# Kernel tuning notes

Measured on AMD Instinct MI355X. Metric: run time of the kernel, lower is better.

Reference implementation:

```python
import jax, jax.numpy as jnp
import numpy as np
from jax import lax


def _gelu(x):
    return jax.nn.gelu(x, approximate=False)  # torch nn.GELU default = exact erf


def _ln_cf(x, g, b, eps=1e-6):
    # channels_first LayerNorm over dim 1 (biased variance, as in the source)
    m = x.mean(1, keepdims=True)
    v = ((x - m) ** 2).mean(1, keepdims=True)
    return g[None, :, None, None] * ((x - m) / jnp.sqrt(v + eps)) + b[None, :, None, None]


def _conv1x1(x, w):
    return jnp.einsum('bihw,oi->bohw', x, w[:, :, 0, 0])


def _conv3x3(x, w, d):
    # 3x3 conv, padding=dilation=d, no bias
    return lax.conv_general_dilated(x, w, (1, 1), [(d, d), (d, d)], rhs_dilation=(d, d),
                                    dimension_numbers=('NCHW', 'OIHW', 'NCHW'))


def _forward(x, conv1_w, conv1_b, conv2_w, conv2_b,
             cw_w1, cw_b1, cw_ln_g, cw_ln_b, cw_w2, cw_b2,
             aspp0_w, aspp0_g, aspp0_b, aspp1_w, aspp1_g, aspp1_b,
             aspp2_w, aspp2_g, aspp2_b, aspp3_w, aspp3_g, aspp3_b,
             asppp_w, asppp_g, asppp_b, proj_w, proj_g, proj_b):
    B, C, H, W = x.shape
    # x1 = conv1(x)
    x1 = _conv1x1(x, conv1_w) + conv1_b[None, :, None, None]
    # ChannelWeighting
    avg = x.mean((2, 3))                                    # [B,C]
    mx = x.max((2, 3))
    o = jnp.abs(avg - mx) * avg
    h = o @ cw_w1.T + cw_b1                                 # [B,Cout]
    mu = h.mean(-1, keepdims=True)
    vv = ((h - mu) ** 2).mean(-1, keepdims=True)
    h = cw_ln_g * ((h - mu) / jnp.sqrt(vv + 1e-5)) + cw_ln_b  # nn.LayerNorm eps=1e-5
    s = jax.nn.sigmoid(h @ cw_w2.T + cw_b2)                 # [B,C]
    xc = x * s[:, :, None, None] + x
    # ASPP (dropout in project is identity at eval)
    b0 = _gelu(_ln_cf(_conv1x1(xc, aspp0_w), aspp0_g, aspp0_b))
    b1 = _gelu(_ln_cf(_conv3x3(xc, aspp1_w, 3), aspp1_g, aspp1_b))
    b2 = _gelu(_ln_cf(_conv3x3(xc, aspp2_w, 6), aspp2_g, aspp2_b))
    b3 = _gelu(_ln_cf(_conv3x3(xc, aspp3_w, 9), aspp3_g, aspp3_b))
    gp = xc.mean((2, 3), keepdims=True)                     # AdaptiveAvgPool2d(1)
    bp = _gelu(_ln_cf(_conv1x1(gp, asppp_w), asppp_g, asppp_b))
    bp = jnp.broadcast_to(bp, (B, C, H, W))                 # bilinear 1x1->HxW == broadcast
    cat = jnp.concatenate([b0, b1, b2, b3, bp], axis=1)     # [B,5C,H,W]
    proj = _gelu(_ln_cf(_conv1x1(cat, proj_w), proj_g, proj_b))
    xa = _conv1x1(proj, conv1_w) + conv1_b[None, :, None, None]
    # AttentionModule, batched (redundant discarded Q@attn from source omitted)
    Co = xa.shape[1]
    HW = H * W
    P = x1.reshape(B, Co, HW)
    Q = xa.reshape(B, Co, HW)
    S = jnp.einsum('bcq,bcp->bqp', Q, P) / jnp.sqrt(jnp.asarray(HW, jnp.float32))
    A = jax.nn.softmax(S, axis=-1)                          # softmax over dim=1 of S[q,p] -> p
    L = jnp.einsum('bck,bkj->bcj', P, A).reshape(B, Co, H, W)
    O = L + xa
    return _conv1x1(O, conv2_w) + conv2_b[None, :, None, None]


def setup_inputs() -> dict:
    key = jax.random.key(0)
    ks = jax.random.split(key, 16)
    Cin, Cout, B, H, W = 256, 128, 4, 64, 64

    def nrm(k, shape, fan):
        return jax.random.normal(k, shape, jnp.float32) / np.float32(np.sqrt(fan))

    return {
        'x': jax.random.normal(ks[0], (B, Cin, H, W), jnp.float32),
        'conv1_w': nrm(ks[1], (Cout, Cin, 1, 1), Cin),
        'conv1_b': jnp.zeros((Cout,), jnp.float32),
        'conv2_w': nrm(ks[2], (Cin, Cout, 1, 1), Cout),
        'conv2_b': jnp.zeros((Cin,), jnp.float32),
        'cw_w1': nrm(ks[3], (Cout, Cin), Cin),
        'cw_b1': jnp.zeros((Cout,), jnp.float32),
        'cw_ln_g': jnp.ones((Cout,), jnp.float32),
        'cw_ln_b': jnp.zeros((Cout,), jnp.float32),
        'cw_w2': nrm(ks[4], (Cin, Cout), Cout),
        'cw_b2': jnp.zeros((Cin,), jnp.float32),
        'aspp0_w': nrm(ks[5], (Cin, Cin, 1, 1), Cin),
        'aspp0_g': jnp.ones((Cin,), jnp.float32),
        'aspp0_b': jnp.zeros((Cin,), jnp.float32),
        'aspp1_w': nrm(ks[6], (Cin, Cin, 3, 3), Cin * 9),
        'aspp1_g': jnp.ones((Cin,), jnp.float32),
        'aspp1_b': jnp.zeros((Cin,), jnp.float32),
        'aspp2_w': nrm(ks[7], (Cin, Cin, 3, 3), Cin * 9),
        'aspp2_g': jnp.ones((Cin,), jnp.float32),
        'aspp2_b': jnp.zeros((Cin,), jnp.float32),
        'aspp3_w': nrm(ks[8], (Cin, Cin, 3, 3), Cin * 9),
        'aspp3_g': jnp.ones((Cin,), jnp.float32),
        'aspp3_b': jnp.zeros((Cin,), jnp.float32),
        'asppp_w': nrm(ks[9], (Cin, Cin, 1, 1), Cin),
        'asppp_g': jnp.ones((Cin,), jnp.float32),
        'asppp_b': jnp.zeros((Cin,), jnp.float32),
        'proj_w': nrm(ks[10], (Cin, 5 * Cin, 1, 1), 5 * Cin),
        'proj_g': jnp.ones((Cin,), jnp.float32),
        'proj_b': jnp.zeros((Cin,), jnp.float32),
    }


def reference(x, conv1_w, conv1_b, conv2_w, conv2_b,
              cw_w1, cw_b1, cw_ln_g, cw_ln_b, cw_w2, cw_b2,
              aspp0_w, aspp0_g, aspp0_b, aspp1_w, aspp1_g, aspp1_b,
              aspp2_w, aspp2_g, aspp2_b, aspp3_w, aspp3_g, aspp3_b,
              asppp_w, asppp_g, asppp_b, proj_w, proj_g, proj_b):
    return _forward(x, conv1_w, conv1_b, conv2_w, conv2_b,
                    cw_w1, cw_b1, cw_ln_g, cw_ln_b, cw_w2, cw_b2,
                    aspp0_w, aspp0_g, aspp0_b, aspp1_w, aspp1_g, aspp1_b,
                    aspp2_w, aspp2_g, aspp2_b, aspp3_w, aspp3_g, aspp3_b,
                    asppp_w, asppp_g, asppp_b, proj_w, proj_g, proj_b)
```

## Files before the change

kernel.cpp:

```cpp
#include <hip/hip_runtime.h>
#include <hip/hip_bf16.h>
#include <math.h>

#define NB 4
#define CI 256
#define CO 128
#define HW 4096

typedef __attribute__((ext_vector_type(8))) short s8v;
typedef __attribute__((ext_vector_type(4))) short s4v;
typedef __attribute__((ext_vector_type(4))) float f4v;

__device__ __forceinline__ unsigned short f2bf(float f){
    __hip_bfloat16 h = __float2bfloat16(f);
    return *reinterpret_cast<unsigned short*>(&h);
}

__device__ __forceinline__ void lds_dma16(const void* g, void* l){
    __builtin_amdgcn_global_load_lds((const __attribute__((address_space(1))) unsigned int*)g,
                                     (__attribute__((address_space(3))) unsigned int*)l,
                                     16, 0, 0);
}

__device__ __forceinline__ float gelu_f(float x){
    float z  = x * 0.70710678118654752f;
    float az = fabsf(z);
    float tt = 1.f / (1.f + 0.3275911f * az);
    float poly = tt*(0.254829592f + tt*(-0.284496736f + tt*(1.421413741f +
                 tt*(-1.453152027f + tt*1.061405429f))));
    float erfv = 1.f - poly * __expf(-az*az);
    erfv = (z < 0.f) ? -erfv : erfv;
    return 0.5f * x * (1.f + erfv);
}

__global__ void k_pre(const float* __restrict__ x, float* __restrict__ avg, float* __restrict__ mx,
                      const float* __restrict__ c1, const float* __restrict__ a0,
                      const float* __restrict__ pj, const float* __restrict__ c2,
                      const float* __restrict__ d3, const float* __restrict__ d6,
                      const float* __restrict__ d9,
                      unsigned short* __restrict__ w_c1, unsigned short* __restrict__ w_a0,
                      unsigned short* __restrict__ w_pj, unsigned short* __restrict__ w_c2,
                      unsigned short* __restrict__ w_d3, unsigned short* __restrict__ w_d6,
                      unsigned short* __restrict__ w_d9){
    int blk = blockIdx.x;
    int t = threadIdx.x;
    if (blk < 1024){
        const float* p = x + (long long)blk * HW;
        float s = 0.f, m = -1e30f;
        for (int i = t; i < HW; i += 256){ float v = p[i]; s += v; m = fmaxf(m, v); }
        __shared__ float ss[256], sm[256];
        ss[t] = s; sm[t] = m; __syncthreads();
        for (int o = 128; o > 0; o >>= 1){
            if (t < o){ ss[t] += ss[t+o]; sm[t] = fmaxf(sm[t], sm[t+o]); }
            __syncthreads();
        }
        if (t == 0){ avg[blk] = ss[0] / (float)HW; mx[blk] = sm[0]; }
        return;
    }
    int i = (blk - 1024)*256 + t;
    if (i < 458752){
        if (i < 32768)        w_c1[i]        = f2bf(c1[i]);
        else if (i < 98304)   w_a0[i-32768]  = f2bf(a0[i-32768]);
        else if (i < 425984)  w_pj[i-98304]  = f2bf(pj[i-98304]);
        else                  w_c2[i-425984] = f2bf(c2[i-425984]);
    } else {
        int j = i - 458752;
        int which = j / 589824;
        int l = j - which*589824;
        int tap = l >> 16, rem = l & 65535, o = rem >> 8, ci = rem & 255;
        const float* src = (which==0) ? d3 : ((which==1) ? d6 : d9);
        unsigned short* dst = (which==0) ? w_d3 : ((which==1) ? w_d6 : w_d9);
        dst[l] = f2bf(src[o*2304 + ci*9 + tap]);
    }
}

__global__ void k_cw(const float* __restrict__ avg, const float* __restrict__ mx,
                     const float* __restrict__ w1, const float* __restrict__ b1,
                     const float* __restrict__ lng, const float* __restrict__ lnb,
                     const float* __restrict__ w2, const float* __restrict__ b2,
                     float* __restrict__ sv, float* __restrict__ gp,
                     float* __restrict__ zb){
    int b = blockIdx.x, t = threadIdx.x;
    if (b == 0) zb[t] = 0.f;
    __shared__ float o_s[256];
    __shared__ float h_s[128];
    __shared__ float stat[2];
    float a = avg[b*256 + t];
    o_s[t] = fabsf(a - mx[b*256 + t]) * a;
    __syncthreads();
    if (t < 128){
        float h = b1[t];
        for (int i = 0; i < 256; i++) h += o_s[i] * w1[t*256 + i];
        h_s[t] = h;
    }
    __syncthreads();
    if (t == 0){
        float s = 0.f, s2 = 0.f;
        for (int j = 0; j < 128; j++){ s += h_s[j]; s2 += h_s[j]*h_s[j]; }
        float mean = s / 128.f;
        float var  = s2 / 128.f - mean*mean;
        stat[0] = mean; stat[1] = rsqrtf(var + 1e-5f);
    }
    __syncthreads();
    if (t < 128) h_s[t] = lng[t] * ((h_s[t] - stat[0]) * stat[1]) + lnb[t];
    __syncthreads();
    float z = b2[t];
    for (int j = 0; j < 128; j++) z += h_s[j] * w2[t*128 + j];
    float sig = 1.f / (1.f + __expf(-z));
    sv[b*256 + t] = sig;
    gp[b*256 + t] = a * (1.f + sig);
}

__global__ void k_xT(const float* __restrict__ x, const float* __restrict__ sv,
                     unsigned short* __restrict__ xT, unsigned short* __restrict__ xcT){
    int b = blockIdx.z, c0 = blockIdx.y*64, h0 = blockIdx.x*64;
    __shared__ unsigned short T1[64][66], T2[64][66];
    int t = threadIdx.x;
    int hl = t & 63, cs = t >> 6;
    #pragma unroll
    for (int r = 0; r < 16; r++){
        int c = cs*16 + r;
        float v = x[((long long)b*256 + c0 + c)*HW + h0 + hl];
        float sc = 1.f + sv[b*256 + c0 + c];
        T1[c][hl] = f2bf(v);
        T2[c][hl] = f2bf(v*sc);
    }
    __syncthreads();
    int cl = t & 63, hs = t >> 6;
    #pragma unroll
    for (int r = 0; r < 16; r++){
        int h = hs*16 + r;
        long long o = ((long long)b*HW + h0 + h)*256 + c0 + cl;
        xT[o]  = T1[cl][h];
        xcT[o] = T2[cl][h];
    }
}

__device__ __forceinline__ void ln_epi32(f4v acc[2][2],
        int b, int n0, int w, int lane, int m, int q, int t,
        const float* Gs, const float* Bts,
        float (*Psum)[32], float (*Psq)[32], float* Mn, float* Iv,
        unsigned short* __restrict__ outT, int outPitch, int colOff){
    float ls[2], ls2[2];
    #pragma unroll
    for (int ct = 0; ct < 2; ct++){
        float s = 0.f, s2 = 0.f;
        #pragma unroll
        for (int ms = 0; ms < 2; ms++)
            #pragma unroll
            for (int r = 0; r < 4; r++){ float v = acc[ms][ct][r]; s += v; s2 += v*v; }
        ls[ct] = s; ls2[ct] = s2;
    }
    #pragma unroll
    for (int ct = 0; ct < 2; ct++){
        ls[ct]  += __shfl_xor(ls[ct], 16);  ls[ct]  += __shfl_xor(ls[ct], 32);
        ls2[ct] += __shfl_xor(ls2[ct], 16); ls2[ct] += __shfl_xor(ls2[ct], 32);
    }
    if (lane < 16){
        #pragma unroll
        for (int ct = 0; ct < 2; ct++){ Psum[w][ct*16+lane] = ls[ct]; Psq[w][ct*16+lane] = ls2[ct]; }
    }
    __syncthreads();
    if (t < 32){
        float s = 0.f, s2 = 0.f;
        #pragma unroll
        for (int ww = 0; ww < 8; ww++){ s += Psum[ww][t]; s2 += Psq[ww][t]; }
        float mean = s * (1.f/256.f);
        Mn[t] = mean;
        Iv[t] = rsqrtf(s2*(1.f/256.f) - mean*mean + 1e-6f);
    }
    __syncthreads();
    #pragma unroll
    for (int ct = 0; ct < 2; ct++){
        int p = ct*16 + m;
        float mean = Mn[p], inv = Iv[p];
        long long rowb = ((long long)b*HW + n0 + p)*outPitch + colOff;
        #pragma unroll
        for (int ms = 0; ms < 2; ms++){
            s4v o4;
            #pragma unroll
            for (int r = 0; r < 4; r++){
                int c = w*32 + ms*16 + q*4 + r;
                float h = Gs[c]*((acc[ms][ct][r] - mean)*inv) + Bts[c];
                o4[r] = (short)f2bf(gelu_f(h));
            }
            *(s4v*)(outT + rowb + w*32 + ms*16 + q*4) = o4;
        }
    }
}

__global__ __launch_bounds__(512, 4)
void k_aspp(const unsigned short* __restrict__ w_a0, const unsigned short* __restrict__ w_d3,
            const unsigned short* __restrict__ w_d6, const unsigned short* __restrict__ w_d9,
            const unsigned short* __restrict__ BT,
            const float* __restrict__ a0_g, const float* __restrict__ a0_b,
            const float* __restrict__ a1_g, const float* __restrict__ a1_b,
            const float* __restrict__ a2_g, const float* __restrict__ a2_b,
            const float* __restrict__ a3_g, const float* __restrict__ a3_b,
            const float* __restrict__ gp, const float* __restrict__ ap_w,
            const float* __restrict__ ap_g, const float* __restrict__ ap_b,
            const float* __restrict__ zbuf,
            unsigned short* __restrict__ catT){
    int br = blockIdx.y, b = blockIdx.z;
    int t = threadIdx.x;
    __shared__ __align__(16) unsigned short As[256*64];
    __shared__ __align__(16) unsigned short Bs[128*64];
    __shared__ float Gs[256], Bts[256];
    if (br == 4){
        int p0 = blockIdx.x*128;
        float* z_s = (float*)As;
        unsigned short* bp_s = As + 2048;
        float* stat = (float*)(As + 4096);
        if (t < 256){
            float z = 0.f;
            for (int c = 0; c < 256; c++) z += gp[b*256 + c] * ap_w[t*256 + c];
            z_s[t] = z;
        }
        __syncthreads();
        if (t == 0){
            float s = 0.f, s2 = 0.f;
            for (int c = 0; c < 256; c++){ s += z_s[c]; s2 += z_s[c]*z_s[c]; }
            float mean = s / 256.f, var = s2 / 256.f - mean*mean;
            stat[0] = mean; stat[1] = rsqrtf(var + 1e-6f);
        }
        __syncthreads();
        if (t < 256){
            float h = ap_g[t] * ((z_s[t] - stat[0]) * stat[1]) + ap_b[t];
            bp_s[t] = f2bf(gelu_f(h));
        }
        __syncthreads();
        for (int it = 0; it < 8; it++){
            int i = it*512 + t;
            int pl = i >> 5, cj = (i & 31) * 8;
            s8v v8;
            #pragma unroll
            for (int k2 = 0; k2 < 8; k2++) v8[k2] = (short)bp_s[cj + k2];
            *(s8v*)(catT + ((long long)b*HW + p0 + pl)*1280 + 1024 + cj) = v8;
        }
        return;
    }
    int n0 = blockIdx.x * 128;
    const unsigned short* BTb = BT + (long long)b*HW*256;
    const unsigned short* A  = (br==0) ? w_a0 : (br==1) ? w_d3 : (br==2) ? w_d6 : w_d9;
    const float* g   = (br==0) ? a0_g : (br==1) ? a1_g : (br==2) ? a2_g : a3_g;
    const float* bta = (br==0) ? a0_b : (br==1) ? a1_b : (br==2) ? a2_b : a3_b;
    int d    = (br==0) ? 0 : (br==1) ? 3 : (br==2) ? 6 : 9;
    int NS   = (br==0) ? 4 : 36;
    if (t < 256){ Gs[t] = g[t]; Bts[t] = bta[t]; }

    int w = t>>6, lane = t&63, m = lane&15, q = lane>>4;
    int wr = w>>1, wc = w&1;
    int rsw = m&7;
    int rl8 = lane>>3;
    int gch = (lane&7) ^ rl8;
    int aoff = rl8*256 + gch*8;
    int y0 = n0 >> 6;

    f4v acc[4][4];
    #pragma unroll
    for (int ms = 0; ms < 4; ms++)
        #pragma unroll
        for (int ct = 0; ct < 4; ct++){ f4v z = {0.f,0.f,0.f,0.f}; acc[ms][ct] = z; }

    for (int s = 0; s < NS; ++s){
        int tap = s>>2, kc = s&3;
        int dy = tap/3 - 1, dx = tap%3 - 1;
        const unsigned short* abase = A + tap*65536 + kc*64 + aoff;
        #pragma unroll
        for (int i = 0; i < 4; i++){
            int row0 = w*32 + i*8;
            lds_dma16(abase + row0*256, &As[row0*64]);
        }
        int xadd = rl8 + dx*d;
        #pragma unroll
        for (int i = 0; i < 2; i++){
            int bn0 = w*16 + i*8;
            int yy = y0 + (bn0>>6) + dy*d;
            int xs = (bn0 & 63) + xadd;
            const unsigned short* gsrc = ((unsigned)yy < 64u && (unsigned)xs < 64u)
                ? (BTb + (long long)(yy*64 + xs)*256 + kc*64 + gch*8)
                : (const unsigned short*)zbuf;
            lds_dma16(gsrc, &Bs[bn0*64]);
        }
        __syncthreads();
        #pragma unroll
        for (int ks = 0; ks < 2; ks++){
            s8v bfr[4];
            #pragma unroll
            for (int ct = 0; ct < 4; ct++)
                bfr[ct] = *(const s8v*)&Bs[(wc*64 + ct*16 + m)*64 + ((q + 4*ks) ^ rsw)*8];
            #pragma unroll
            for (int ms = 0; ms < 4; ms++){
                s8v afr = *(const s8v*)&As[(wr*64 + ms*16 + m)*64 + ((q + 4*ks) ^ rsw)*8];
                #pragma unroll
                for (int ct = 0; ct < 4; ct++)
                    acc[ms][ct] = __builtin_amdgcn_mfma_f32_16x16x32_bf16(afr, bfr[ct], acc[ms][ct], 0,0,0);
            }
        }
        __syncthreads();
    }
    float* Psum = (float*)Bs;
    float* Psq  = Psum + 512;
    float* Mn   = Psq  + 512;
    float* Iv   = Mn   + 128;
    #pragma unroll
    for (int ct = 0; ct < 4; ct++){
        float s = 0.f, s2 = 0.f;
        #pragma unroll
        for (int ms = 0; ms < 4; ms++)
            #pragma unroll
            for (int r = 0; r < 4; r++){ float v = acc[ms][ct][r]; s += v; s2 += v*v; }
        s  += __shfl_xor(s, 16);  s  += __shfl_xor(s, 32);
        s2 += __shfl_xor(s2, 16); s2 += __shfl_xor(s2, 32);
        if (lane < 16){
            Psum[wr*128 + wc*64 + ct*16 + lane] = s;
            Psq [wr*128 + wc*64 + ct*16 + lane] = s2;
        }
    }
    __syncthreads();
    if (t < 128){
        float s  = Psum[t] + Psum[128+t] + Psum[256+t] + Psum[384+t];
        float s2 = Psq [t] + Psq [128+t] + Psq [256+t] + Psq [384+t];
        float mean = s * (1.f/256.f);
        Mn[t] = mean;
        Iv[t] = rsqrtf(s2*(1.f/256.f) - mean*mean + 1e-6f);
    }
    __syncthreads();
    #pragma unroll
    for (int ct = 0; ct < 4; ct++){
        int p = wc*64 + ct*16 + m;
        float mean = Mn[p], inv = Iv[p];
        long long rowb = ((long long)b*HW + n0 + p)*1280 + br*256;
        #pragma unroll
        for (int ms = 0; ms < 4; ms++){
            s4v o4;
            #pragma unroll
            for (int r = 0; r < 4; r++){
                int c = wr*64 + ms*16 + q*4 + r;
                float h = Gs[c]*((acc[ms][ct][r] - mean)*inv) + Bts[c];
                o4[r] = (short)f2bf(gelu_f(h));
            }
            *(s4v*)(catT + rowb + wr*64 + ms*16 + q*4) = o4;
        }
    }
}

__global__ __launch_bounds__(512)
void k_branch1(const unsigned short* __restrict__ A, int K,
               const unsigned short* __restrict__ BT,
               const float* __restrict__ g, const float* __restrict__ beta,
               unsigned short* __restrict__ outT, int outPitch, int colOff){
    int b = blockIdx.y, n0 = blockIdx.x*32;
    const unsigned short* BTb = BT + (long long)b*HW*K;
    __shared__ unsigned short As[256][72];
    __shared__ unsigned short Bs[32][72];
    __shared__ float Psum[8][32], Psq[8][32], Mn[32], Iv[32];
    __shared__ float Gs[256], Bts[256];
    int t = threadIdx.x, w = t>>6, lane = t&63, m = lane&15, q = lane>>4;
    if (t < 256){ Gs[t] = g[t]; Bts[t] = beta[t]; }
    f4v acc[2][2];
    #pragma unroll
    for (int ms = 0; ms < 2; ms++)
        #pragma unroll
        for (int ct = 0; ct < 2; ct++){ f4v z = {0.f,0.f,0.f,0.f}; acc[ms][ct] = z; }
    for (int k0 = 0; k0 < K; k0 += 64){
        __syncthreads();
        {   int r = t>>1, half = t&1;
            const uint4* src = (const uint4*)(A + (long long)r*K + k0 + half*32);
            uint4* dst = (uint4*)&As[r][half*32];
            dst[0]=src[0]; dst[1]=src[1]; dst[2]=src[2]; dst[3]=src[3];
        }
        {   int n = t>>4, ch = t&15;
            *(uint2*)&Bs[n][ch*4] = *(const uint2*)(BTb + (long long)(n0+n)*K + k0 + ch*4);
        }
        __syncthreads();
        #pragma unroll
        for (int ks = 0; ks < 2; ks++){
            s8v bfr[2];
            #pragma unroll
            for (int ct = 0; ct < 2; ct++) bfr[ct] = *(const s8v*)&Bs[ct*16+m][q*8+ks*32];
            #pragma unroll
            for (int ms = 0; ms < 2; ms++){
                s8v afr = *(const s8v*)&As[w*32 + ms*16 + m][q*8+ks*32];
                #pragma unroll
                for (int ct = 0; ct < 2; ct++)
                    acc[ms][ct] = __builtin_amdgcn_mfma_f32_16x16x32_bf16(afr, bfr[ct], acc[ms][ct], 0,0,0);
            }
        }
    }
    __syncthreads();
    ln_epi32(acc, b, n0, w, lane, m, q, t, Gs, Bts, Psum, Psq, Mn, Iv, outT, outPitch, colOff);
}

__global__ __launch_bounds__(256)
void k_conv1m(const unsigned short* __restrict__ A,
              const unsigned short* __restrict__ BT,
              const float* __restrict__ bias,
              unsigned short* __restrict__ outT,
              unsigned short* __restrict__ outC,
              float* __restrict__ outF){
    int b = blockIdx.y, n0 = blockIdx.x*32;
    const unsigned short* BTb = BT + (long long)b*HW*256;
    __shared__ unsigned short As[128][72];
    __shared__ unsigned short Bs[32][72];
    int t = threadIdx.x, w = t>>6, lane = t&63, m = lane&15, q = lane>>4;
    f4v acc[2][2];
    #pragma unroll
    for (int ms = 0; ms < 2; ms++)
        #pragma unroll
        for (int ct = 0; ct < 2; ct++){ f4v z = {0.f,0.f,0.f,0.f}; acc[ms][ct] = z; }
    for (int k0 = 0; k0 < 256; k0 += 64){
        __syncthreads();
        {   int r = t>>1, half = t&1;
            const uint4* src = (const uint4*)(A + (long long)r*256 + k0 + half*32);
            uint4* dst = (uint4*)&As[r][half*32];
            dst[0]=src[0]; dst[1]=src[1]; dst[2]=src[2]; dst[3]=src[3];
        }
        {   int n = t>>3, ch = t&7;
            *(uint4*)&Bs[n][ch*8] = *(const uint4*)(BTb + (long long)(n0+n)*256 + k0 + ch*8);
        }
        __syncthreads();
        #pragma unroll
        for (int ks = 0; ks < 2; ks++){
            s8v bfr[2];
            #pragma unroll
            for (int ct = 0; ct < 2; ct++) bfr[ct] = *(const s8v*)&Bs[ct*16+m][q*8+ks*32];
            #pragma unroll
            for (int ms = 0; ms < 2; ms++){
                s8v afr = *(const s8v*)&As[w*32 + ms*16 + m][q*8+ks*32];
                #pragma unroll
                for (int ct = 0; ct < 2; ct++)
                    acc[ms][ct] = __builtin_amdgcn_mfma_f32_16x16x32_bf16(afr, bfr[ct], acc[ms][ct], 0,0,0);
            }
        }
    }
    #pragma unroll
    for (int ct = 0; ct < 2; ct++){
        int p = n0 + ct*16 + m;
        #pragma unroll
        for (int ms = 0; ms < 2; ms++){
            s4v o4;
            float vals[4];
            #pragma unroll
            for (int r = 0; r < 4; r++){
                int c = w*32 + ms*16 + q*4 + r;
                vals[r] = acc[ms][ct][r] + bias[c];
                o4[r] = (short)f2bf(vals[r]);
            }
            *(s4v*)(outT + ((long long)b*HW + p)*128 + w*32 + ms*16 + q*4) = o4;
            if (outC){
                #pragma unroll
                for (int r = 0; r < 4; r++){
                    int c = w*32 + ms*16 + q*4 + r;
                    outC[((long long)b*128 + c)*HW + p] = (unsigned short)o4[r];
                }
            }
            if (outF){
                #pragma unroll
                for (int r = 0; r < 4; r++){
                    int c = w*32 + ms*16 + q*4 + r;
                    outF[((long long)b*128 + c)*HW + p] = vals[r];
                }
            }
        }
    }
}

__global__ __launch_bounds__(256)
void k_attn_stats3(const unsigned short* __restrict__ QT,
                   const unsigned short* __restrict__ PT,
                   float* __restrict__ lpart){
    int b = blockIdx.z, jc = blockIdx.y, k0 = blockIdx.x * 128;
    const unsigned short* QTb = QT + (long long)b * HW * CO;
    const unsigned short* PTb = PT + (long long)b * HW * CO;
    __shared__ unsigned short Ps[2][64][132];
    int t = threadIdx.x;
    int w = t >> 6, lane = t & 63, m = lane & 15, q = lane >> 4;
    s8v a[2][4];
    #pragma unroll
    for (int kh = 0; kh < 2; kh++)
        #pragma unroll
        for (int ks = 0; ks < 4; ks++)
            a[kh][ks] = *(const s8v*)(QTb + (long long)(k0 + kh*64 + w*16 + m) * CO + q*8 + ks*32);
    float rl[2][4];
    #pragma unroll
    for (int kh = 0; kh < 2; kh++)
        #pragma unroll
        for (int r = 0; r < 4; r++) rl[kh][r] = 0.f;
    const float scale = 0.015625f;
    int jbase = jc * 1024;
    int sr = t >> 2, sch = t & 3;
    uint4 pf[4];
    {   const uint4* src = (const uint4*)(PTb + (long long)(jbase + sr) * CO + sch * 32);
        #pragma unroll
        for (int i = 0; i < 4; i++) pf[i] = src[i];
    }
    for (int jt = 0; jt < 16; jt++){
        int cur = jt & 1;
        {   uint4* dst = (uint4*)&Ps[cur][sr][sch * 32];
            #pragma unroll
            for (int i = 0; i < 4; i++) dst[i] = pf[i];
        }
        __syncthreads();
        if (jt < 15){
            const uint4* src = (const uint4*)(PTb + (long long)(jbase + (jt+1)*64 + sr) * CO + sch * 32);
            #pragma unroll
            for (int i = 0; i < 4; i++) pf[i] = src[i];
        }
        #pragma unroll
        for (int kh = 0; kh < 2; kh++){
            float sv[4][4];
            #pragma unroll
            for (int ct = 0; ct < 4; ct++){
                f4v acc = {0.f,0.f,0.f,0.f};
                #pragma unroll
                for (int ks = 0; ks < 4; ks++){
                    s8v bv = *(const s8v*)&Ps[cur][ct*16 + m][q*8 + ks*32];
                    acc = __builtin_amdgcn_mfma_f32_16x16x32_bf16(a[kh][ks], bv, acc, 0, 0, 0);
                }
                #pragma unroll
                for (int r = 0; r < 4; r++) sv[ct][r] = acc[r] * scale;
            }
            #pragma unroll
            for (int r = 0; r < 4; r++){
                float se = __expf(sv[0][r]) + __expf(sv[1][r])
                         + __expf(sv[2][r]) + __expf(sv[3][r]);
                #pragma unroll
                for (int msk = 1; msk < 16; msk <<= 1) se += __shfl_xor(se, msk);
                rl[kh][r] += se;
            }
        }
    }
    if (m == 0){
        #pragma unroll
        for (int kh = 0; kh < 2; kh++)
            #pragma unroll
            for (int r = 0; r < 4; r++){
                int k = k0 + kh*64 + w*16 + q*4 + r;
                lpart[(long long)jc * (NB*HW) + (long long)b*HW + k] = rl[kh][r];
            }
    }
}

__global__ __launch_bounds__(256)
void k_attn_apply2(const unsigned short* __restrict__ QT,
                   const unsigned short* __restrict__ PT,
                   const unsigned short* __restrict__ Pb,
                   const float* __restrict__ lpart,
                   float* __restrict__ Lp){
    int b = blockIdx.z, kc = blockIdx.y, j0 = blockIdx.x * 64;
    const unsigned short* QTb = QT + (long long)b * HW * CO;
    const unsigned short* PTb = PT + (long long)b * HW * CO;
    const unsigned short* Pbb = Pb + (long long)b * CO * HW;
    __shared__ unsigned short Qks[64][136];
    __shared__ unsigned short Pcs[128][72];
    __shared__ unsigned short Et[64][72];
    __shared__ float Il[1024];
    int t = threadIdx.x;
    int w = t >> 6, lane = t & 63, m = lane & 15, q = lane >> 4;
    int kbase = kc * 1024;
    {
        #pragma unroll
        for (int r = 0; r < 4; r++){
            int kl = t*4 + r;
            long long gi = (long long)b*HW + kbase + kl;
            float l = lpart[gi] + lpart[gi+16384] + lpart[gi+32768] + lpart[gi+49152];
            Il[kl] = 1.f / l;
        }
    }
    {
        int r = t >> 2, ch = t & 3;
        const uint4* src = (const uint4*)(PTb + (long long)(j0 + r) * CO + ch * 32);
        uint4* dst = (uint4*)&Qks[r][ch * 32];
        #pragma unroll
        for (int i = 0; i < 4; i++) dst[i] = src[i];
    }
    __syncthreads();
    s8v bj[4][4];
    #pragma unroll
    for (int ct = 0; ct < 4; ct++)
        #pragma unroll
        for (int ks = 0; ks < 4; ks++)
            bj[ct][ks] = *(const s8v*)&Qks[ct*16 + m][q*8 + ks*32];
    f4v accL[2][4];
    #pragma unroll
    for (int mt = 0; mt < 2; mt++)
        #pragma unroll
        for (int ct = 0; ct < 4; ct++){ f4v z = {0.f,0.f,0.f,0.f}; accL[mt][ct] = z; }
    const float scale = 0.015625f;
    for (int kt = 0; kt < 16; kt++){
        int k0 = kbase + kt*64;
        __syncthreads();
        {
            int r = t >> 2, ch = t & 3;
            const uint4* src = (const uint4*)(QTb + (long long)(k0 + r) * CO + ch * 32);
            uint4* dst = (uint4*)&Qks[r][ch * 32];
            #pragma unroll
            for (int i = 0; i < 4; i++) dst[i] = src[i];
        }
        {
            int c = t >> 1, hf = t & 1;
            const uint4* src = (const uint4*)(Pbb + (long long)c * HW + k0 + hf * 32);
            uint4* dst = (uint4*)&Pcs[c][hf * 32];
            #pragma unroll
            for (int i = 0; i < 4; i++) dst[i] = src[i];
        }
        __syncthreads();
        s8v aS[4];
        #pragma unroll
        for (int ks = 0; ks < 4; ks++) aS[ks] = *(const s8v*)&Qks[w*16 + m][q*8 + ks*32];
        float il[4];
        #pragma unroll
        for (int r = 0; r < 4; r++) il[r] = Il[kt*64 + w*16 + q*4 + r];
        #pragma unroll
        for (int ct = 0; ct < 4; ct++){
            f4v s = {0.f,0.f,0.f,0.f};
            #pragma unroll
            for (int ks = 0; ks < 4; ks++)
                s = __builtin_amdgcn_mfma_f32_16x16x32_bf16(aS[ks], bj[ct][ks], s, 0, 0, 0);
            s4v e4;
            #pragma unroll
            for (int r = 0; r < 4; r++)
                e4[r] = (short)f2bf(__expf(s[r]*scale) * il[r]);
            *(s4v*)&Et[ct*16 + m][w*16 + q*4] = e4;
        }
        __syncthreads();
        s8v aP[2][2];
        #pragma unroll
        for (int mt = 0; mt < 2; mt++)
            #pragma unroll
            for (int ks2 = 0; ks2 < 2; ks2++)
                aP[mt][ks2] = *(const s8v*)&Pcs[w*32 + mt*16 + m][q*8 + ks2*32];
        #pragma unroll
        for (int ct = 0; ct < 4; ct++){
            s8v bE0 = *(const s8v*)&Et[ct*16 + m][q*8];
            s8v bE1 = *(const s8v*)&Et[ct*16 + m][q*8 + 32];
            #pragma unroll
            for (int mt = 0; mt < 2; mt++){
                accL[mt][ct] = __builtin_amdgcn_mfma_f32_16x16x32_bf16(aP[mt][0], bE0, accL[mt][ct], 0, 0, 0);
                accL[mt][ct] = __builtin_amdgcn_mfma_f32_16x16x32_bf16(aP[mt][1], bE1, accL[mt][ct], 0, 0, 0);
            }
        }
    }
    float* Lpb = Lp + ((long long)(kc*NB + b) * CO) * HW;
    #pragma unroll
    for (int mt = 0; mt < 2; mt++)
        #pragma unroll
        for (int ct = 0; ct < 4; ct++)
            #pragma unroll
            for (int r = 0; r < 4; r++){
                int c = w*32 + mt*16 + q*4 + r;
                Lpb[(long long)c*HW + j0 + ct*16 + m] = accL[mt][ct][r];
            }
}

__global__ __launch_bounds__(256)
void k_outfused(const unsigned short* __restrict__ A,
                const float* __restrict__ Lp, const float* __restrict__ xa,
                const float* __restrict__ bias, float* __restrict__ out){
    int b = blockIdx.y, j0 = blockIdx.x*32;
    __shared__ unsigned short Bs[32][136];
    __shared__ __align__(16) char pool[256*68*2];
    int t = threadIdx.x;
    {
        float* Bsf = (float*)pool;
        int c = t>>1, jh = t&1;
        long long base = ((long long)b*CO + c)*HW + j0 + jh*16;
        const long long csz = (long long)NB*CO*HW;
        float v[16];
        #pragma unroll
        for (int r = 0; r < 16; r++) v[r] = xa[base + r];
        #pragma unroll
        for (int pidx = 0; pidx < 4; pidx++){
            const float* src = Lp + pidx*csz + base;
            #pragma unroll
            for (int r = 0; r < 16; r++) v[r] += src[r];
        }
        #pragma unroll
        for (int r = 0; r < 16; r++) Bsf[c*33 + jh*16 + r] = v[r];
    }
    __syncthreads();
    {
        const float* Bsf = (const float*)pool;
        int j = t>>3, cs = t&7;
        #pragma unroll
        for (int r = 0; r < 16; r++){
            int c = cs*16 + r;
            Bs[j][c] = f2bf(Bsf[c*33 + j]);
        }
    }
    __syncthreads();
    unsigned short (*As)[68] = (unsigned short(*)[68])pool;
    int w = t>>6, lane = t&63, m = lane&15, q = lane>>4;
    f4v acc[4][2];
    #pragma unroll
    for (int ms = 0; ms < 4; ms++)
        #pragma unroll
        for (int ct = 0; ct < 2; ct++){ f4v z = {0.f,0.f,0.f,0.f}; acc[ms][ct] = z; }
    for (int k0 = 0; k0 < 128; k0 += 64){
        __syncthreads();
        {   const uint4* src = (const uint4*)(A + (long long)t*128 + k0);
            uint4* dst = (uint4*)&As[t][0];
            #pragma unroll
            for (int i = 0; i < 8; i++) dst[i] = src[i];
        }
        __syncthreads();
        #pragma unroll
        for (int ks = 0; ks < 2; ks++){
            s8v bfr[2];
            #pragma unroll
            for (int ct = 0; ct < 2; ct++) bfr[ct] = *(const s8v*)&Bs[ct*16+m][k0 + ks*32 + q*8];
            #pragma unroll
            for (int ms = 0; ms < 4; ms++){
                s8v afr = *(const s8v*)&As[w*64 + ms*16 + m][q*8 + ks*32];
                #pragma unroll
                for (int ct = 0; ct < 2; ct++)
                    acc[ms][ct] = __builtin_amdgcn_mfma_f32_16x16x32_bf16(afr, bfr[ct], acc[ms][ct], 0,0,0);
            }
        }
    }
    #pragma unroll
    for (int ct = 0; ct < 2; ct++){
        int p = j0 + ct*16 + m;
        #pragma unroll
        for (int ms = 0; ms < 4; ms++)
            #pragma unroll
            for (int r = 0; r < 4; r++){
                int c = w*64 + ms*16 + q*4 + r;
                out[((long long)b*256 + c)*HW + p] = acc[ms][ct][r] + bias[c];
            }
    }
}

extern "C" void kernel_launch(void* const* d_in, const int* in_sizes, int n_in,
                              void* d_out, int out_size, void* d_ws, size_t ws_size,
                              hipStream_t stream) {
    const float* x       = (const float*)d_in[0];
    const float* conv1_w = (const float*)d_in[1];
    const float* conv1_b = (const float*)d_in[2];
    const float* conv2_w = (const float*)d_in[3];
    const float* conv2_b = (const float*)d_in[4];
    const float* cw_w1   = (const float*)d_in[5];
    const float* cw_b1   = (const float*)d_in[6];
    const float* cw_g    = (const float*)d_in[7];
    const float* cw_bt   = (const float*)d_in[8];
    const float* cw_w2   = (const float*)d_in[9];
    const float* cw_b2   = (const float*)d_in[10];
    const float* a0_w    = (const float*)d_in[11];
    const float* a0_g    = (const float*)d_in[12];
    const float* a0_b    = (const float*)d_in[13];
    const float* a1_w    = (const float*)d_in[14];
    const float* a1_g    = (const float*)d_in[15];
    const float* a1_b    = (const float*)d_in[16];
    const float* a2_w    = (const float*)d_in[17];
    const float* a2_g    = (const float*)d_in[18];
    const float* a2_b    = (const float*)d_in[19];
    const float* a3_w    = (const float*)d_in[20];
    const float* a3_g    = (const float*)d_in[21];
    const float* a3_b    = (const float*)d_in[22];
    const float* ap_w    = (const float*)d_in[23];
    const float* ap_g    = (const float*)d_in[24];
    const float* ap_b    = (const float*)d_in[25];
    const float* pj_w    = (const float*)d_in[26];
    const float* pj_g    = (const float*)d_in[27];
    const float* pj_b    = (const float*)d_in[28];
    float* out = (float*)d_out;

    float* ws    = (float*)d_ws;
    float* avg   = ws;
    float* mx    = ws + 1024;
    float* sv    = ws + 2048;
    float* gp    = ws + 3072;
    float* zbuf  = ws + 4096;
    float* xa    = ws + 37888;
    float* lpart = xa + 2097152;
    unsigned short* sb = (unsigned short*)(ws + 4232192);
    unsigned short* xT    = sb;
    unsigned short* xcT   = sb + 4194304;
    unsigned short* catT  = sb + 8388608;
    unsigned short* projT = sb + 29360128;
    unsigned short* P_bf  = sb + 33554432;
    unsigned short* PT_bf = sb + 35651584;
    unsigned short* QT_bf = sb + 37748736;
    unsigned short* w_c1  = sb + 41943040;
    unsigned short* w_a0  = sb + 41975808;
    unsigned short* w_pj  = sb + 42041344;
    unsigned short* w_c2  = sb + 42369024;
    unsigned short* w_d3  = sb + 42401792;
    unsigned short* w_d6  = sb + 42991616;
    unsigned short* w_d9  = sb + 43581440;
    float* Lp = (float*)catT;

    k_pre<<<dim3(9728), 256, 0, stream>>>(x, avg, mx,
                                          conv1_w, a0_w, pj_w, conv2_w, a1_w, a2_w, a3_w,
                                          w_c1, w_a0, w_pj, w_c2, w_d3, w_d6, w_d9);
    k_cw<<<dim3(NB), 256, 0, stream>>>(avg, mx, cw_w1, cw_b1, cw_g, cw_bt, cw_w2, cw_b2, sv, gp, zbuf);

    k_xT<<<dim3(64, 4, NB), 256, 0, stream>>>(x, sv, xT, xcT);

    k_conv1m<<<dim3(128, NB), 256, 0, stream>>>(w_c1, xT, conv1_b, PT_bf, P_bf, nullptr);

    k_aspp<<<dim3(32, 5, NB), 512, 0, stream>>>(w_a0, w_d3, w_d6, w_d9, xcT,
                                                a0_g, a0_b, a1_g, a1_b, a2_g, a2_b, a3_g, a3_b,
                                                gp, ap_w, ap_g, ap_b, zbuf, catT);

    k_branch1<<<dim3(128, NB), 512, 0, stream>>>(w_pj, 1280, catT, pj_g, pj_b, projT, 256, 0);

    k_conv1m<<<dim3(128, NB), 256, 0, stream>>>(w_c1, projT, conv1_b, QT_bf, nullptr, xa);

    k_attn_stats3<<<dim3(32, 4, NB), 256, 0, stream>>>(QT_bf, PT_bf, lpart);
    k_attn_apply2<<<dim3(64, 4, NB), 256, 0, stream>>>(QT_bf, PT_bf, P_bf, lpart, Lp);

    k_outfused<<<dim3(128, NB), 256, 0, stream>>>(w_c2, Lp, xa, conv2_b, out);

    (void)in_sizes; (void)n_in; (void)out_size; (void)ws_size;
}
```

Before: 410.9 us.

## Triple-buffer ASPP conv K-loop with async LDS DMA and halved K-step

The ASPP GEMM main loop goes from a single-buffered 64-wide K step with two full barriers per iteration to a three-slot ring of 32-wide K steps. Loads for step h+2 are issued before computing step h, with a partial vmcnt wait and a single raw s_barrier per step. This is meant to hide global-to-LDS latency behind the MFMA work. Branch order is also remapped so the heavy dilated-conv branches get the low blockIdx.y values and the light 1x1 branch comes last, which should improve tail scheduling. In exchange the loop has twice as many iterations and barriers, uses more LDS (which may lower occupancy), and relies on a hand-written waitcnt count being correct.

```diff
diff --git a/kernel.cpp b/kernel.cpp
--- a/kernel.cpp
+++ b/kernel.cpp
@@ -203,14 +203,13 @@
             unsigned short* __restrict__ catT){
     int br = blockIdx.y, b = blockIdx.z;
     int t = threadIdx.x;
-    __shared__ __align__(16) unsigned short As[256*64];
-    __shared__ __align__(16) unsigned short Bs[128*64];
+    __shared__ __align__(16) unsigned short SB[3][12288];
     __shared__ float Gs[256], Bts[256];
     if (br == 4){
         int p0 = blockIdx.x*128;
-        float* z_s = (float*)As;
-        unsigned short* bp_s = As + 2048;
-        float* stat = (float*)(As + 4096);
+        float* z_s = (float*)&SB[0][0];
+        unsigned short* bp_s = &SB[0][2048];
+        float* stat = (float*)&SB[0][4096];
         if (t < 256){
             float z = 0.f;
             for (int c = 0; c < 256; c++) z += gp[b*256 + c] * ap_w[t*256 + c];
@@ -241,20 +240,23 @@
     }
     int n0 = blockIdx.x * 128;
     const unsigned short* BTb = BT + (long long)b*HW*256;
-    const unsigned short* A  = (br==0) ? w_a0 : (br==1) ? w_d3 : (br==2) ? w_d6 : w_d9;
-    const float* g   = (br==0) ? a0_g : (br==1) ? a1_g : (br==2) ? a2_g : a3_g;
-    const float* bta = (br==0) ? a0_b : (br==1) ? a1_b : (br==2) ? a2_b : a3_b;
-    int d    = (br==0) ? 0 : (br==1) ? 3 : (br==2) ? 6 : 9;
-    int NS   = (br==0) ? 4 : 36;
+    const unsigned short* A  = (br==0) ? w_d3 : (br==1) ? w_d6 : (br==2) ? w_d9 : w_a0;
+    const float* g   = (br==0) ? a1_g : (br==1) ? a2_g : (br==2) ? a3_g : a0_g;
+    const float* bta = (br==0) ? a1_b : (br==1) ? a2_b : (br==2) ? a3_b : a0_b;
+    int d    = (br==0) ? 3 : (br==1) ? 6 : (br==2) ? 9 : 0;
+    int slot = (br==3) ? 0 : (br+1);
+    int HS   = (br==3) ? 8 : 72;
     if (t < 256){ Gs[t] = g[t]; Bts[t] = bta[t]; }
 
     int w = t>>6, lane = t&63, m = lane&15, q = lane>>4;
     int wr = w>>1, wc = w&1;
-    int rsw = m&7;
-    int rl8 = lane>>3;
-    int gch = (lane&7) ^ rl8;
-    int aoff = rl8*256 + gch*8;
+    int dr = lane>>2;
+    int dchunk = (lane&3) ^ (dr&3);
+    int aoffL = dr*256 + dchunk*8 + (w*32)*256;
+    int browL = w*16 + dr;
+    int bxL = browL & 63, byL = browL >> 6;
     int y0 = n0 >> 6;
+    int roff = (q ^ (m&3))*8;
 
     f4v acc[4][4];
     #pragma unroll
@@ -262,44 +264,49 @@
         #pragma unroll
         for (int ct = 0; ct < 4; ct++){ f4v z = {0.f,0.f,0.f,0.f}; acc[ms][ct] = z; }
 
-    for (int s = 0; s < NS; ++s){
-        int tap = s>>2, kc = s&3;
-        int dy = tap/3 - 1, dx = tap%3 - 1;
-        const unsigned short* abase = A + tap*65536 + kc*64 + aoff;
-        #pragma unroll
-        for (int i = 0; i < 4; i++){
-            int row0 = w*32 + i*8;
-            lds_dma16(abase + row0*256, &As[row0*64]);
-        }
-        int xadd = rl8 + dx*d;
-        #pragma unroll
-        for (int i = 0; i < 2; i++){
-            int bn0 = w*16 + i*8;
-            int yy = y0 + (bn0>>6) + dy*d;
-            int xs = (bn0 & 63) + xadd;
-            const unsigned short* gsrc = ((unsigned)yy < 64u && (unsigned)xs < 64u)
-                ? (BTb + (long long)(yy*64 + xs)*256 + kc*64 + gch*8)
-                : (const unsigned short*)zbuf;
-            lds_dma16(gsrc, &Bs[bn0*64]);
-        }
-        __syncthreads();
-        #pragma unroll
-        for (int ks = 0; ks < 2; ks++){
+    auto stage = [&](int h, unsigned short* dst){
+        int tap = h>>3, kc = h&7;
+        int dy = tap/3 - 1, dx = tap - (tap/3)*3 - 1;
+        const unsigned short* asrc = A + tap*65536 + kc*32 + aoffL;
+        lds_dma16(asrc,          dst + w*32*32);
+        lds_dma16(asrc + 16*256, dst + (w*32+16)*32);
+        int ys = y0 + byL + dy*d;
+        int xs = bxL + dx*d;
+        const unsigned short* bsrc = ((unsigned)ys < 64u && (unsigned)xs < 64u)
+            ? (BTb + (long long)((ys<<6) + xs)*256 + kc*32 + dchunk*8)
+            : (const unsigned short*)zbuf;
+        lds_dma16(bsrc, dst + 8192 + w*16*32);
+    };
+
+    stage(0, SB[0]);
+    stage(1, SB[1]);
+    asm volatile("s_waitcnt vmcnt(3)" ::: "memory");
+    __builtin_amdgcn_s_barrier();
+    __builtin_amdgcn_sched_barrier(0);
+    unsigned short *pc = SB[0], *pn = SB[1], *pf = SB[2];
+    for (int h = 0; h < HS; ++h){
+        if (h+2 < HS) stage(h+2, pf);
+        #pragma unroll
+        for (int ks = 0; ks < 1; ks++){
             s8v bfr[4];
             #pragma unroll
             for (int ct = 0; ct < 4; ct++)
-                bfr[ct] = *(const s8v*)&Bs[(wc*64 + ct*16 + m)*64 + ((q + 4*ks) ^ rsw)*8];
+                bfr[ct] = *(const s8v*)&pc[8192 + (wc*64 + ct*16 + m)*32 + roff];
             #pragma unroll
             for (int ms = 0; ms < 4; ms++){
-                s8v afr = *(const s8v*)&As[(wr*64 + ms*16 + m)*64 + ((q + 4*ks) ^ rsw)*8];
+                s8v afr = *(const s8v*)&pc[(wr*64 + ms*16 + m)*32 + roff];
                 #pragma unroll
                 for (int ct = 0; ct < 4; ct++)
                     acc[ms][ct] = __builtin_amdgcn_mfma_f32_16x16x32_bf16(afr, bfr[ct], acc[ms][ct], 0,0,0);
             }
         }
-        __syncthreads();
-    }
-    float* Psum = (float*)Bs;
+        if (h+2 < HS) { asm volatile("s_waitcnt vmcnt(3)" ::: "memory"); }
+        else          { asm volatile("s_waitcnt vmcnt(0)" ::: "memory"); }
+        __builtin_amdgcn_s_barrier();
+        __builtin_amdgcn_sched_barrier(0);
+        unsigned short* tmp = pc; pc = pn; pn = pf; pf = tmp;
+    }
+    float* Psum = (float*)&SB[0][0];
     float* Psq  = Psum + 512;
     float* Mn   = Psq  + 512;
     float* Iv   = Mn   + 128;
@@ -330,7 +337,7 @@
     for (int ct = 0; ct < 4; ct++){
         int p = wc*64 + ct*16 + m;
         float mean = Mn[p], inv = Iv[p];
-        long long rowb = ((long long)b*HW + n0 + p)*1280 + br*256;
+        long long rowb = ((long long)b*HW + n0 + p)*1280 + slot*256;
         #pragma unroll
         for (int ms = 0; ms < 4; ms++){
             s4v o4;
```

Result: no change. 416.1 us (+1.3%).
